# Kernel optimization log

Measured on AMD Instinct MI355X. Metric: run time of the kernel, lower is better.

## Reference

```python
import jax, jax.numpy as jnp
import numpy as np

DIM = 64
N = 10000
E = 40000


def setup_inputs() -> dict:
    key = jax.random.key(0)
    ks = jax.random.split(key, 16)
    def rn(k, shape, s):
        return jax.random.normal(k, shape, dtype=jnp.float32) * s
    inp = {}
    inp["x"] = jax.random.normal(ks[0], (N, 3), dtype=jnp.float32)
    inp["edge_attr"] = jax.random.uniform(ks[1], (E, 7), dtype=jnp.float32)
    inp["edge_index"] = jax.random.randint(ks[2], (2, E), 0, N)
    inp["batch"] = jnp.zeros((N,), dtype=jnp.int32)
    # lin0: Linear(3, dim)
    inp["lin0_w"] = rn(ks[3], (DIM, 3), 0.3)
    inp["lin0_b"] = jnp.zeros((DIM,), jnp.float32)
    # edge MLP: Linear(7, dim) -> ReLU -> Linear(dim, dim*dim)
    inp["em1_w"] = rn(ks[4], (DIM, 7), 0.3)
    inp["em1_b"] = jnp.zeros((DIM,), jnp.float32)
    inp["em2_w"] = rn(ks[5], (DIM * DIM, DIM), 0.05)
    inp["em2_b"] = jnp.zeros((DIM * DIM,), jnp.float32)
    # NNConv root weight [in, out] and bias
    inp["root_w"] = rn(ks[6], (DIM, DIM), 0.1)
    inp["conv_b"] = jnp.zeros((DIM,), jnp.float32)
    # GRU(dim, dim), gate order r, z, n
    inp["gru_wih"] = rn(ks[7], (3 * DIM, DIM), 0.1)
    inp["gru_whh"] = rn(ks[8], (3 * DIM, DIM), 0.1)
    inp["gru_bih"] = jnp.zeros((3 * DIM,), jnp.float32)
    inp["gru_bhh"] = jnp.zeros((3 * DIM,), jnp.float32)
    # Set2Set LSTM(2*dim, dim), gate order i, f, g, o
    inp["lstm_wih"] = rn(ks[9], (4 * DIM, 2 * DIM), 0.1)
    inp["lstm_whh"] = rn(ks[10], (4 * DIM, DIM), 0.1)
    inp["lstm_bih"] = jnp.zeros((4 * DIM,), jnp.float32)
    inp["lstm_bhh"] = jnp.zeros((4 * DIM,), jnp.float32)
    inp["lin1_w"] = rn(ks[11], (DIM, 2 * DIM), 0.1)
    inp["lin1_b"] = jnp.zeros((DIM,), jnp.float32)
    inp["lin3_w"] = rn(ks[12], (1, DIM), 0.1)
    inp["lin3_b"] = jnp.zeros((1,), jnp.float32)
    return inp


def _forward(x, edge_attr, lin0_w, lin0_b, em1_w, em1_b, em2_w, em2_b,
             root_w, conv_b, gru_wih, gru_whh, gru_bih, gru_bhh,
             lstm_wih, lstm_whh, lstm_bih, lstm_bhh,
             lin1_w, lin1_b, lin3_w, lin3_b, edge_index, batch):
    n = x.shape[0]
    dim = lin0_w.shape[0]
    src, dst = edge_index[0], edge_index[1]

    out = jax.nn.relu(x @ lin0_w.T + lin0_b)  # [N, dim]
    h = out                                   # GRU hidden state

    # Edge-conditioned weights depend only on edge_attr -> compute once.
    we = jax.nn.relu(edge_attr @ em1_w.T + em1_b) @ em2_w.T + em2_b
    we = we.reshape(-1, dim, dim)             # [E, dim, dim]

    deg = jax.ops.segment_sum(jnp.ones_like(src, dtype=x.dtype), dst, num_segments=n)
    inv_deg = jnp.where(deg > 0, 1.0 / jnp.maximum(deg, 1.0), 0.0)[:, None]

    for _ in range(6):
        # NNConv: per-edge matmul, scatter-mean, plus root transform
        msg = jnp.einsum('ei,eio->eo', out[src], we)            # [E, dim]
        agg = jax.ops.segment_sum(msg, dst, num_segments=n) * inv_deg
        m = jax.nn.relu(out @ root_w + agg + conv_b)            # [N, dim]
        # single-step GRU over nodes (seq_len=1, batch=N)
        gi = m @ gru_wih.T + gru_bih
        gh = h @ gru_whh.T + gru_bhh
        ir, iz, inew = jnp.split(gi, 3, axis=-1)
        hr, hz, hnew = jnp.split(gh, 3, axis=-1)
        r = jax.nn.sigmoid(ir + hr)
        z = jax.nn.sigmoid(iz + hz)
        ncand = jnp.tanh(inew + r * hnew)
        h = (1.0 - z) * ncand + z * h
        out = h

    # Set2Set pooling; single graph (batch is all zeros, pool.view(1,-1))
    q_star = jnp.zeros((1, 2 * dim), x.dtype)
    hl = jnp.zeros((1, dim), x.dtype)
    cl = jnp.zeros((1, dim), x.dtype)
    for _ in range(6):
        g = q_star @ lstm_wih.T + lstm_bih + hl @ lstm_whh.T + lstm_bhh
        gi_, gf_, gg_, go_ = jnp.split(g, 4, axis=-1)
        cl = jax.nn.sigmoid(gf_) * cl + jax.nn.sigmoid(gi_) * jnp.tanh(gg_)
        hl = jax.nn.sigmoid(go_) * jnp.tanh(cl)
        q = hl                                                  # [1, dim]
        e = jnp.einsum('nd,d->n', out, q[0])                    # attention logits
        a = jax.nn.softmax(e)                                   # softmax over the single graph
        r = jnp.einsum('n,nd->d', a, out)[None, :]              # readout [1, dim]
        q_star = jnp.concatenate([q, r], axis=-1)               # [1, 2*dim]

    pool = q_star.reshape(1, -1)
    hid = jax.nn.relu(pool @ lin1_w.T + lin1_b)
    return hid @ lin3_w.T + lin3_b                              # [1, 1]


def reference(x, edge_attr, edge_index, batch, lin0_w, lin0_b, em1_w, em1_b,
              em2_w, em2_b, root_w, conv_b, gru_wih, gru_whh, gru_bih, gru_bhh,
              lstm_wih, lstm_whh, lstm_bih, lstm_bhh, lin1_w, lin1_b, lin3_w, lin3_b):
    return _forward(x, edge_attr, lin0_w, lin0_b, em1_w, em1_b, em2_w, em2_b,
                    root_w, conv_b, gru_wih, gru_whh, gru_bih, gru_bhh,
                    lstm_wih, lstm_whh, lstm_bih, lstm_bhh,
                    lin1_w, lin1_b, lin3_w, lin3_b, edge_index, batch)
```

## Files before the change

### kernel.cpp

```cpp
#include <hip/hip_runtime.h>
#include <math.h>

#define NNODES 10000
#define NEDGES 40000
#define DIM 64
#define MC 4160
#define WS 200
#define AST2 72

typedef short bf16x8 __attribute__((ext_vector_type(8)));
typedef float floatx4 __attribute__((ext_vector_type(4)));

__device__ __forceinline__ float sigmoidf_(float x) { return 1.0f / (1.0f + expf(-x)); }

__device__ __forceinline__ unsigned short f2bf(float x) {
    unsigned int u = __float_as_uint(x);
    u += 0x7fffu + ((u >> 16) & 1u);
    return (unsigned short)(u >> 16);
}
__device__ __forceinline__ float bf2f(unsigned short h) {
    return __uint_as_float(((unsigned int)h) << 16);
}
__device__ __forceinline__ void write_split(unsigned short* __restrict__ p, int d, float v) {
    unsigned short hi = f2bf(v);
    unsigned short lo = f2bf(v - bf2f(hi));
    p[d] = hi;
    p[64 + d] = hi;
    p[128 + d] = lo;
}

__global__ __launch_bounds__(256) void k_prep(const float* __restrict__ x,
                                              const float* __restrict__ lin0_w,
                                              const float* __restrict__ lin0_b,
                                              float* __restrict__ out,
                                              unsigned short* __restrict__ Abf,
                                              const float* __restrict__ em2_w,
                                              const float* __restrict__ em2_b,
                                              unsigned short* __restrict__ Bbf,
                                              const float* __restrict__ root_w,
                                              const float* __restrict__ gwih,
                                              const float* __restrict__ gwhh,
                                              unsigned short* __restrict__ Wcat,
                                              const float* __restrict__ lwih,
                                              const float* __restrict__ lwhh,
                                              float* __restrict__ wcT,
                                              float* __restrict__ wrT,
                                              const int* __restrict__ ei,
                                              int* __restrict__ counts,
                                              float* __restrict__ deg) {
    const int b = blockIdx.x;
    const int tid = threadIdx.x;
    if (b < 2500) {
        int idx = b * 256 + tid;
        if (idx >= NNODES * 64) return;
        int n = idx >> 6, d = idx & 63;
        float a = lin0_b[d];
        a += x[n * 3 + 0] * lin0_w[d * 3 + 0];
        a += x[n * 3 + 1] * lin0_w[d * 3 + 1];
        a += x[n * 3 + 2] * lin0_w[d * 3 + 2];
        float v = fmaxf(a, 0.0f);
        out[idx] = v;
        write_split(Abf + (size_t)n * 192, d, v);
    } else if (b < 3540) {
        int idx = (b - 2500) * 256 + tid;
        if (idx >= 64 * MC) return;
        int c = idx >> 6, i = idx & 63;
        float v;
        if (c < 4096) {
            v = em2_w[((size_t)(i * 64 + (c >> 6))) * 64 + (c & 63)];
        } else {
            v = em2_b[i * 64 + (c - 4096)];
        }
        unsigned short hi = f2bf(v);
        unsigned short lo = f2bf(v - bf2f(hi));
        unsigned short* row = Bbf + (size_t)c * 192;
        row[i] = hi;
        row[64 + i] = lo;
        row[128 + i] = hi;
    } else if (b < 3652) {
        int idx = (b - 3540) * 256 + tid;
        if (idx >= 448 * 64) return;
        int r = idx >> 6, i = idx & 63;
        float v;
        if (r < 64) v = root_w[i * 64 + r];
        else if (r < 256) v = gwih[(r - 64) * 64 + i];
        else v = gwhh[(r - 256) * 64 + i];
        unsigned short hi = f2bf(v);
        unsigned short lo = f2bf(v - bf2f(hi));
        unsigned short* row = Wcat + (size_t)r * 192;
        row[i] = hi;
        row[64 + i] = lo;
        row[128 + i] = hi;
    } else if (b < 3780) {
        int idx = (b - 3652) * 256 + tid;
        if (idx < 64 * 256) {
            int k = idx >> 8, t = idx & 255;
            wcT[idx] = lwih[t * 128 + k] + lwhh[t * 64 + k];
        } else if (idx < 2 * 64 * 256) {
            int i2 = idx - 64 * 256;
            int k = i2 >> 8, t = i2 & 255;
            wrT[i2] = lwih[t * 128 + 64 + k];
        }
    } else {
        int e = (b - 3780) * 256 + tid;
        if (e < NEDGES) {
            atomicAdd(&counts[ei[e]], 1);
            atomicAdd(&deg[ei[NEDGES + e]], 1.0f);
        }
    }
}

__global__ __launch_bounds__(256) void k_scan(const int* __restrict__ counts,
                                              const float* __restrict__ deg,
                                              int* __restrict__ row_start,
                                              int* __restrict__ cursor,
                                              float* __restrict__ invd) {
    __shared__ int partial[256];
    const int tid = threadIdx.x;
    const int base = tid * 40;
    int local[40];
    int sum = 0;
#pragma unroll
    for (int i = 0; i < 40; ++i) {
        int idx = base + i;
        int v = (idx < NNODES) ? counts[idx] : 0;
        local[i] = sum;
        sum += v;
    }
    partial[tid] = sum;
    __syncthreads();
    for (int off = 1; off < 256; off <<= 1) {
        int t = (tid >= off) ? partial[tid - off] : 0;
        __syncthreads();
        partial[tid] += t;
        __syncthreads();
    }
    const int prev = (tid > 0) ? partial[tid - 1] : 0;
#pragma unroll
    for (int i = 0; i < 40; ++i) {
        int idx = base + i;
        if (idx < NNODES) {
            int rs = prev + local[i];
            row_start[idx] = rs;
            cursor[idx] = rs;
            float dg = deg[idx];
            invd[idx] = dg > 0.0f ? 1.0f / dg : 0.0f;
        }
    }
    if (tid == 255) row_start[NNODES] = partial[255];
}

__global__ __launch_bounds__(256) void k_edge(const int* __restrict__ ei,
                                              const float* __restrict__ ea,
                                              const float* __restrict__ w,
                                              const float* __restrict__ bvec,
                                              int* __restrict__ cursor,
                                              int* __restrict__ dst_s,
                                              float* __restrict__ h1s) {
    const int wv = threadIdx.x >> 6, lane = threadIdx.x & 63;
    const int e = blockIdx.x * 4 + wv;
    if (e >= NEDGES) return;
    int pos = 0;
    if (lane == 0) {
        int s = ei[e];
        pos = atomicAdd(&cursor[s], 1);
        dst_s[pos] = ei[NEDGES + e];
    }
    pos = __shfl(pos, 0);
    float a = bvec[lane];
#pragma unroll
    for (int j = 0; j < 7; ++j) a += ea[e * 7 + j] * w[lane * 7 + j];
    h1s[(size_t)pos * 64 + lane] = fmaxf(a, 0.0f);
}

__global__ __launch_bounds__(256) void k_gemmM(const unsigned short* __restrict__ Abf,
                                               const unsigned short* __restrict__ Bbf,
                                               unsigned short* __restrict__ Mb) {
    __shared__ __align__(16) unsigned short As[64 * AST2];
    __shared__ __align__(16) unsigned short Bs[64 * AST2];
    __shared__ __align__(16) float Cs[64 * 68];
    const int tid = threadIdx.x;
    const int col0 = blockIdx.x * 64;
    const int wave = tid >> 6, lane = tid & 63;
    const int mi = lane & 15, q = lane >> 4;
#pragma unroll
    for (int j = 0; j < 2; ++j) {
        int idx = tid + 256 * j;
        int r = idx >> 3, c8 = (idx & 7) * 8;
        *reinterpret_cast<uint4*>(&Bs[r * AST2 + c8]) =
            *reinterpret_cast<const uint4*>(&Bbf[(size_t)(col0 + r) * 192 + c8]);
    }
    for (int rt = 0; rt < 4; ++rt) {
        const int row0 = (blockIdx.y * 4 + rt) * 64;
#pragma unroll
        for (int j = 0; j < 2; ++j) {
            int idx = tid + 256 * j;
            int r = idx >> 3, c8 = (idx & 7) * 8;
            int ra = row0 + r;
            if (ra >= NNODES) ra = NNODES - 1;
            *reinterpret_cast<uint4*>(&As[r * AST2 + c8]) =
                *reinterpret_cast<const uint4*>(&Abf[(size_t)ra * 192 + c8]);
        }
        __syncthreads();
        floatx4 acc[4];
#pragma unroll
        for (int nt = 0; nt < 4; ++nt)
#pragma unroll
            for (int r = 0; r < 4; ++r) acc[nt][r] = 0.0f;
        const unsigned short* arow = &As[(wave * 16 + mi) * AST2 + q * 8];
#pragma unroll
        for (int ks = 0; ks < 2; ++ks) {
            bf16x8 a = *reinterpret_cast<const bf16x8*>(arow + ks * 32);
#pragma unroll
            for (int nt = 0; nt < 4; ++nt) {
                bf16x8 b = *reinterpret_cast<const bf16x8*>(&Bs[(nt * 16 + mi) * AST2 + ks * 32 + q * 8]);
                acc[nt] = __builtin_amdgcn_mfma_f32_16x16x32_bf16(a, b, acc[nt], 0, 0, 0);
            }
        }
        const int rl = wave * 16 + q * 4;
#pragma unroll
        for (int nt = 0; nt < 4; ++nt)
#pragma unroll
            for (int r = 0; r < 4; ++r)
                Cs[(rl + r) * 68 + nt * 16 + mi] = acc[nt][r];
        __syncthreads();
#pragma unroll
        for (int j = 0; j < 2; ++j) {
            int idx = tid + 256 * j;
            int r = idx >> 3, c8 = (idx & 7) * 8;
            int row = row0 + r;
            if (row < NNODES) {
                const float* src = &Cs[r * 68 + c8];
                unsigned int p0 = (unsigned int)f2bf(src[0]) | ((unsigned int)f2bf(src[1]) << 16);
                unsigned int p1 = (unsigned int)f2bf(src[2]) | ((unsigned int)f2bf(src[3]) << 16);
                unsigned int p2 = (unsigned int)f2bf(src[4]) | ((unsigned int)f2bf(src[5]) << 16);
                unsigned int p3 = (unsigned int)f2bf(src[6]) | ((unsigned int)f2bf(src[7]) << 16);
                *reinterpret_cast<uint4*>(&Mb[(size_t)row * MC + col0 + c8]) =
                    make_uint4(p0, p1, p2, p3);
            }
        }
        __syncthreads();
    }
}

__global__ __launch_bounds__(256) void k_msg(const unsigned short* __restrict__ Mb,
                                             const float* __restrict__ h1s,
                                             const int* __restrict__ row_start,
                                             const int* __restrict__ dst_s,
                                             float* __restrict__ agg) {
    const int w = threadIdx.x >> 6;
    const int o = threadIdx.x & 63;
    const int s = blockIdx.x * 4 + w;
    const int e0 = row_start[s], e1 = row_start[s + 1];
    if (e0 == e1) return;
    const unsigned short* mrow = Mb + (size_t)s * MC + o * 64;
    uint4 m[8];
#pragma unroll
    for (int j = 0; j < 8; ++j)
        m[j] = *reinterpret_cast<const uint4*>(mrow + j * 8);
    const float bias = bf2f(Mb[(size_t)s * MC + 4096 + o]);
    for (int e = e0; e < e1; ++e) {
        const float4* hv = reinterpret_cast<const float4*>(h1s + (size_t)e * 64);
        float acc = bias;
#pragma unroll
        for (int j = 0; j < 8; ++j) {
            float4 ha = hv[2 * j];
            float4 hb = hv[2 * j + 1];
            unsigned int u;
            u = m[j].x;
            acc += ha.x * __uint_as_float(u << 16) + ha.y * __uint_as_float(u & 0xffff0000u);
            u = m[j].y;
            acc += ha.z * __uint_as_float(u << 16) + ha.w * __uint_as_float(u & 0xffff0000u);
            u = m[j].z;
            acc += hb.x * __uint_as_float(u << 16) + hb.y * __uint_as_float(u & 0xffff0000u);
            u = m[j].w;
            acc += hb.z * __uint_as_float(u << 16) + hb.w * __uint_as_float(u & 0xffff0000u);
        }
        atomicAdd(&agg[(size_t)dst_s[e] * 64 + o], acc);
    }
}

__global__ __launch_bounds__(256) void k_node(float* __restrict__ agg,
                                              const float* __restrict__ invdeg,
                                              const unsigned short* __restrict__ Wcat,
                                              const float* __restrict__ conv_b,
                                              const float* __restrict__ bih,
                                              const float* __restrict__ bhh,
                                              float* __restrict__ out,
                                              unsigned short* __restrict__ Abf) {
    __shared__ unsigned short As[32 * WS];
    __shared__ unsigned short Ms[32 * WS];
    __shared__ float ho[32 * 68];
    const int tid = threadIdx.x;
    const int row0 = blockIdx.x * 32;
#pragma unroll
    for (int j = 0; j < 3; ++j) {
        int idx = tid + 256 * j;
        int r = idx / 24, jj = idx % 24;
        int ra = row0 + r; if (ra >= NNODES) ra = NNODES - 1;
        *reinterpret_cast<uint4*>(&As[r * WS + jj * 8]) =
            *reinterpret_cast<const uint4*>(&Abf[(size_t)ra * 192 + jj * 8]);
    }
#pragma unroll
    for (int j = 0; j < 2; ++j) {
        int idx = tid + 256 * j;
        int r = idx >> 4, c4 = (idx & 15) * 4;
        int ra = row0 + r; if (ra >= NNODES) ra = NNODES - 1;
        *reinterpret_cast<float4*>(&ho[r * 68 + c4]) =
            *reinterpret_cast<const float4*>(&out[(size_t)ra * 64 + c4]);
    }
    __syncthreads();
    const int wave = tid >> 6, lane = tid & 63;
    const int mi = lane & 15, q = lane >> 4;
    const int d = wave * 16 + mi;
    floatx4 gh[2][3];
#pragma unroll
    for (int rt = 0; rt < 2; ++rt)
#pragma unroll
        for (int g = 0; g < 3; ++g)
#pragma unroll
            for (int r = 0; r < 4; ++r) gh[rt][g][r] = 0.0f;
#pragma unroll
    for (int ks = 0; ks < 6; ++ks) {
        bf16x8 b[3];
#pragma unroll
        for (int g = 0; g < 3; ++g)
            b[g] = *reinterpret_cast<const bf16x8*>(&Wcat[(size_t)(256 + g * 64 + d) * 192 + ks * 32 + q * 8]);
#pragma unroll
        for (int rt = 0; rt < 2; ++rt) {
            bf16x8 a = *reinterpret_cast<const bf16x8*>(&As[(rt * 16 + mi) * WS + ks * 32 + q * 8]);
#pragma unroll
            for (int g = 0; g < 3; ++g)
                gh[rt][g] = __builtin_amdgcn_mfma_f32_16x16x32_bf16(a, b[g], gh[rt][g], 0, 0, 0);
        }
    }
    {
        floatx4 cm[2];
#pragma unroll
        for (int rt = 0; rt < 2; ++rt)
#pragma unroll
            for (int r = 0; r < 4; ++r) cm[rt][r] = 0.0f;
#pragma unroll
        for (int ks = 0; ks < 6; ++ks) {
            bf16x8 b = *reinterpret_cast<const bf16x8*>(&Wcat[(size_t)d * 192 + ks * 32 + q * 8]);
#pragma unroll
            for (int rt = 0; rt < 2; ++rt) {
                bf16x8 a = *reinterpret_cast<const bf16x8*>(&As[(rt * 16 + mi) * WS + ks * 32 + q * 8]);
                cm[rt] = __builtin_amdgcn_mfma_f32_16x16x32_bf16(a, b, cm[rt], 0, 0, 0);
            }
        }
        const float cb = conv_b[d];
#pragma unroll
        for (int rt = 0; rt < 2; ++rt) {
#pragma unroll
            for (int r = 0; r < 4; ++r) {
                int row = rt * 16 + q * 4 + r;
                int ra = row0 + row; int rc = (ra < NNODES) ? ra : NNODES - 1;
                float v = cm[rt][r] + agg[(size_t)rc * 64 + d] * invdeg[rc] + cb;
                if (ra < NNODES) agg[(size_t)ra * 64 + d] = 0.0f;
                v = fmaxf(v, 0.0f);
                unsigned short hi = f2bf(v);
                unsigned short lo = f2bf(v - bf2f(hi));
                Ms[row * WS + d] = hi;
                Ms[row * WS + 64 + d] = hi;
                Ms[row * WS + 128 + d] = lo;
            }
        }
    }
    __syncthreads();
    floatx4 gi[2][3];
#pragma unroll
    for (int rt = 0; rt < 2; ++rt)
#pragma unroll
        for (int g = 0; g < 3; ++g)
#pragma unroll
            for (int r = 0; r < 4; ++r) gi[rt][g][r] = 0.0f;
#pragma unroll
    for (int ks = 0; ks < 6; ++ks) {
        bf16x8 b[3];
#pragma unroll
        for (int g = 0; g < 3; ++g)
            b[g] = *reinterpret_cast<const bf16x8*>(&Wcat[(size_t)(64 + g * 64 + d) * 192 + ks * 32 + q * 8]);
#pragma unroll
        for (int rt = 0; rt < 2; ++rt) {
            bf16x8 a = *reinterpret_cast<const bf16x8*>(&Ms[(rt * 16 + mi) * WS + ks * 32 + q * 8]);
#pragma unroll
            for (int g = 0; g < 3; ++g)
                gi[rt][g] = __builtin_amdgcn_mfma_f32_16x16x32_bf16(a, b[g], gi[rt][g], 0, 0, 0);
        }
    }
    const float bi_r = bih[d], bi_z = bih[64 + d], bi_n = bih[128 + d];
    const float bh_r = bhh[d], bh_z = bhh[64 + d], bh_n = bhh[128 + d];
#pragma unroll
    for (int rt = 0; rt < 2; ++rt) {
#pragma unroll
        for (int r = 0; r < 4; ++r) {
            int row = rt * 16 + q * 4 + r;
            int ra = row0 + row;
            float rr = sigmoidf_(gi[rt][0][r] + bi_r + gh[rt][0][r] + bh_r);
            float zz = sigmoidf_(gi[rt][1][r] + bi_z + gh[rt][1][r] + bh_z);
            float nc = tanhf(gi[rt][2][r] + bi_n + rr * (gh[rt][2][r] + bh_n));
            float hn = (1.0f - zz) * nc + zz * ho[row * 68 + d];
            if (ra < NNODES) {
                out[(size_t)ra * 64 + d] = hn;
                write_split(Abf + (size_t)ra * 192, d, hn);
            }
        }
    }
}

__global__ __launch_bounds__(256) void k_step(const float* __restrict__ out,
                                              const float* __restrict__ wcT,
                                              const float* __restrict__ wrT,
                                              const float* __restrict__ bih,
                                              const float* __restrict__ bhh,
                                              float* __restrict__ hc,
                                              float* rs,
                                              int it) {
    __shared__ float outs[256 * 65];
    __shared__ float hl_s[64];
    __shared__ float qr[64];
    __shared__ float gsh[256];
    __shared__ float wsh[256];
    __shared__ float red[256];
    const int tid = threadIdx.x;
    const int n0 = blockIdx.x * 256;
#pragma unroll
    for (int j = 0; j < 16; ++j) {
        int idx = tid + 256 * j;
        int r = idx >> 4, c4 = (idx & 15) * 4;
        int n = n0 + r;
        float4 v = make_float4(0.0f, 0.0f, 0.0f, 0.0f);
        if (n < NNODES) v = *reinterpret_cast<const float4*>(&out[(size_t)n * 64 + c4]);
        outs[r * 65 + c4 + 0] = v.x;
        outs[r * 65 + c4 + 1] = v.y;
        outs[r * 65 + c4 + 2] = v.z;
        outs[r * 65 + c4 + 3] = v.w;
    }
    if (tid < 64) {
        hl_s[tid] = hc[it * 128 + tid];
        qr[tid] = (it > 0) ? rs[it * 68 + tid] / rs[it * 68 + 64] : 0.0f;
    }
    __syncthreads();
    float g0 = 0.0f, g1 = 0.0f, g2 = 0.0f, g3 = 0.0f;
#pragma unroll 4
    for (int k = 0; k < 64; k += 4) {
        g0 += hl_s[k + 0] * wcT[(k + 0) * 256 + tid] + qr[k + 0] * wrT[(k + 0) * 256 + tid];
        g1 += hl_s[k + 1] * wcT[(k + 1) * 256 + tid] + qr[k + 1] * wrT[(k + 1) * 256 + tid];
        g2 += hl_s[k + 2] * wcT[(k + 2) * 256 + tid] + qr[k + 2] * wrT[(k + 2) * 256 + tid];
        g3 += hl_s[k + 3] * wcT[(k + 3) * 256 + tid] + qr[k + 3] * wrT[(k + 3) * 256 + tid];
    }
    gsh[tid] = bih[tid] + bhh[tid] + ((g0 + g1) + (g2 + g3));
    __syncthreads();
    if (tid < 64) {
        float ig = sigmoidf_(gsh[tid]);
        float fg = sigmoidf_(gsh[64 + tid]);
        float gg = tanhf(gsh[128 + tid]);
        float og = sigmoidf_(gsh[192 + tid]);
        float c = fg * hc[it * 128 + 64 + tid] + ig * gg;
        float h = og * tanhf(c);
        hl_s[tid] = h;
        hc[(it + 1) * 128 + tid] = h;
        hc[(it + 1) * 128 + 64 + tid] = c;
    }
    __syncthreads();
    float w = 0.0f;
    if (n0 + tid < NNODES) {
        const float* row = &outs[tid * 65];
        float e0 = 0.0f, e1 = 0.0f, e2 = 0.0f, e3 = 0.0f;
#pragma unroll 8
        for (int k = 0; k < 64; k += 4) {
            e0 += row[k + 0] * hl_s[k + 0];
            e1 += row[k + 1] * hl_s[k + 1];
            e2 += row[k + 2] * hl_s[k + 2];
            e3 += row[k + 3] * hl_s[k + 3];
        }
        w = expf((e0 + e1) + (e2 + e3));
    }
    wsh[tid] = w;
    red[tid] = w;
    __syncthreads();
    for (int s = 128; s > 0; s >>= 1) {
        if (tid < s) red[tid] += red[tid + s];
        __syncthreads();
    }
    if (tid == 0) atomicAdd(&rs[(it + 1) * 68 + 64], red[0]);
    const int grp = tid >> 6, d = tid & 63;
    float a0 = 0.0f, a1 = 0.0f;
#pragma unroll 8
    for (int j = 0; j < 64; j += 2) {
        a0 += wsh[grp * 64 + j] * outs[(grp * 64 + j) * 65 + d];
        a1 += wsh[grp * 64 + j + 1] * outs[(grp * 64 + j + 1) * 65 + d];
    }
    atomicAdd(&rs[(it + 1) * 68 + d], a0 + a1);
}

__global__ __launch_bounds__(128) void k_out(const float* __restrict__ hc,
                                             const float* __restrict__ rs,
                                             const float* __restrict__ lin1_w,
                                             const float* __restrict__ lin1_b,
                                             const float* __restrict__ lin3_w,
                                             const float* __restrict__ lin3_b,
                                             float* __restrict__ dout) {
    __shared__ float qs[128];
    __shared__ float hs[64];
    int tid = threadIdx.x;
    qs[tid] = (tid < 64) ? hc[6 * 128 + tid] : rs[6 * 68 + (tid - 64)] / rs[6 * 68 + 64];
    __syncthreads();
    if (tid < 64) {
        float a = lin1_b[tid];
        for (int k = 0; k < 128; ++k) a += qs[k] * lin1_w[tid * 128 + k];
        hs[tid] = fmaxf(a, 0.0f);
    }
    __syncthreads();
    if (tid == 0) {
        float a = lin3_b[0];
        for (int k = 0; k < 64; ++k) a += hs[k] * lin3_w[k];
        dout[0] = a;
    }
}

extern "C" void kernel_launch(void* const* d_in, const int* in_sizes, int n_in,
                              void* d_out, int out_size, void* d_ws, size_t ws_size,
                              hipStream_t stream) {
    const float* x         = (const float*)d_in[0];
    const float* edge_attr = (const float*)d_in[1];
    const int*   ei        = (const int*)d_in[2];
    const float* lin0_w    = (const float*)d_in[4];
    const float* lin0_b    = (const float*)d_in[5];
    const float* em1_w     = (const float*)d_in[6];
    const float* em1_b     = (const float*)d_in[7];
    const float* em2_w     = (const float*)d_in[8];
    const float* em2_b     = (const float*)d_in[9];
    const float* root_w    = (const float*)d_in[10];
    const float* conv_b    = (const float*)d_in[11];
    const float* gru_wih   = (const float*)d_in[12];
    const float* gru_whh   = (const float*)d_in[13];
    const float* gru_bih   = (const float*)d_in[14];
    const float* gru_bhh   = (const float*)d_in[15];
    const float* lstm_wih  = (const float*)d_in[16];
    const float* lstm_whh  = (const float*)d_in[17];
    const float* lstm_bih  = (const float*)d_in[18];
    const float* lstm_bhh  = (const float*)d_in[19];
    const float* lin1_w    = (const float*)d_in[20];
    const float* lin1_b    = (const float*)d_in[21];
    const float* lin3_w    = (const float*)d_in[22];
    const float* lin3_b    = (const float*)d_in[23];

    float* ws = (float*)d_ws;
    size_t off = 0;
    unsigned short* Mb   = (unsigned short*)(ws + off); off += (size_t)NNODES * MC / 2;
    unsigned short* Abf  = (unsigned short*)(ws + off); off += (size_t)NNODES * 192 / 2;
    unsigned short* Bbf  = (unsigned short*)(ws + off); off += (size_t)MC * 192 / 2;
    unsigned short* Wcat = (unsigned short*)(ws + off); off += (size_t)448 * 192 / 2;
    float* h1s   = ws + off; off += (size_t)NEDGES * 64;
    float* outb  = ws + off; off += (size_t)NNODES * 64;
    float* agg   = ws + off; off += (size_t)NNODES * 64;
    float* deg   = ws + off; off += NNODES;
    int*   counts    = (int*)(ws + off); off += NNODES;
    int*   cursor    = (int*)(ws + off); off += NNODES;
    int*   row_start = (int*)(ws + off); off += NNODES + 4;
    int*   dst_s     = (int*)(ws + off); off += NEDGES;
    float* invd  = ws + off; off += NNODES;
    float* wcT   = ws + off; off += 64 * 256;
    float* wrT   = ws + off; off += 64 * 256;
    float* rs    = ws + off; off += 7 * 68;
    float* hc    = ws + off; off += 7 * 128;

    hipMemsetAsync(deg, 0, 3 * NNODES * sizeof(float), stream);
    hipMemsetAsync(agg, 0, (size_t)NNODES * 64 * sizeof(float), stream);
    hipMemsetAsync(rs, 0, (7 * 68 + 7 * 128) * sizeof(float), stream);
    k_prep<<<3937, 256, 0, stream>>>(x, lin0_w, lin0_b, outb, Abf,
                                     em2_w, em2_b, Bbf,
                                     root_w, gru_wih, gru_whh, Wcat,
                                     lstm_wih, lstm_whh, wcT, wrT,
                                     ei, counts, deg);
    k_scan<<<1, 256, 0, stream>>>(counts, deg, row_start, cursor, invd);
    k_edge<<<10000, 256, 0, stream>>>(ei, edge_attr, em1_w, em1_b, cursor, dst_s, h1s);

    for (int t = 0; t < 6; ++t) {
        k_gemmM<<<dim3(65, 40), 256, 0, stream>>>(Abf, Bbf, Mb);
        k_msg<<<2500, 256, 0, stream>>>(Mb, h1s, row_start, dst_s, agg);
        k_node<<<313, 256, 0, stream>>>(agg, invd, Wcat, conv_b, gru_bih, gru_bhh,
                                        outb, Abf);
    }

    for (int it = 0; it < 6; ++it)
        k_step<<<40, 256, 0, stream>>>(outb, wcT, wrT, lstm_bih, lstm_bhh, hc, rs, it);
    k_out<<<1, 128, 0, stream>>>(hc, rs, lin1_w, lin1_b, lin3_w, lin3_b, (float*)d_out);
}
```

Measured before the change: 700.3 us.

## Replace node-weight GEMM plus message kernel with fused per-edge outer-product MFMA conv

Instead of precomputing a per-source-node matrix M (N x 4160) via a GEMM and then applying it per edge, each block of 128 edges forms the outer product of the source node feature and the edge hidden vector on the fly as bf16 MFMA A operands. These are multiplied against the em2 weight (plus the bias block) streamed through double-buffered shared memory, and the results are atomically added into agg. This avoids writing and reading the large N x 4160 intermediate every iteration and merges two launches into one. In exchange it does 4x more MFMA work (per edge rather than per node) and drops the hi/lo split precision, using a single bf16 product for inputs and weights.

```diff
diff --git a/kernel.cpp b/kernel.cpp
--- a/kernel.cpp
+++ b/kernel.cpp
@@ -4,9 +4,11 @@
 #define NNODES 10000
 #define NEDGES 40000
 #define DIM 64
-#define MC 4160
 #define WS 200
-#define AST2 72
+#define EB 128
+#define H1S 68
+#define OTS 72
+#define BSS 72
 
 typedef short bf16x8 __attribute__((ext_vector_type(8)));
 typedef float floatx4 __attribute__((ext_vector_type(4)));
@@ -36,7 +38,7 @@
                                               unsigned short* __restrict__ Abf,
                                               const float* __restrict__ em2_w,
                                               const float* __restrict__ em2_b,
-                                              unsigned short* __restrict__ Bbf,
+                                              unsigned short* __restrict__ Bek,
                                               const float* __restrict__ root_w,
                                               const float* __restrict__ gwih,
                                               const float* __restrict__ gwhh,
@@ -63,20 +65,10 @@
         write_split(Abf + (size_t)n * 192, d, v);
     } else if (b < 3540) {
         int idx = (b - 2500) * 256 + tid;
-        if (idx >= 64 * MC) return;
-        int c = idx >> 6, i = idx & 63;
-        float v;
-        if (c < 4096) {
-            v = em2_w[((size_t)(i * 64 + (c >> 6))) * 64 + (c & 63)];
-        } else {
-            v = em2_b[i * 64 + (c - 4096)];
-        }
-        unsigned short hi = f2bf(v);
-        unsigned short lo = f2bf(v - bf2f(hi));
-        unsigned short* row = Bbf + (size_t)c * 192;
-        row[i] = hi;
-        row[64 + i] = lo;
-        row[128 + i] = hi;
+        if (idx >= 4160 * 64) return;
+        int r = idx >> 6, k = idx & 63;
+        float v = (r < 4096) ? em2_w[(size_t)r * 64 + k] : em2_b[k * 64 + (r - 4096)];
+        Bek[idx] = f2bf(v);
     } else if (b < 3652) {
         int idx = (b - 3540) * 256 + tid;
         if (idx >= 448 * 64) return;
@@ -155,6 +147,7 @@
                                               const float* __restrict__ w,
                                               const float* __restrict__ bvec,
                                               int* __restrict__ cursor,
+                                              int* __restrict__ src_s,
                                               int* __restrict__ dst_s,
                                               float* __restrict__ h1s) {
     const int wv = threadIdx.x >> 6, lane = threadIdx.x & 63;
@@ -164,6 +157,7 @@
     if (lane == 0) {
         int s = ei[e];
         pos = atomicAdd(&cursor[s], 1);
+        src_s[pos] = s;
         dst_s[pos] = ei[NEDGES + e];
     }
     pos = __shfl(pos, 0);
@@ -173,110 +167,90 @@
     h1s[(size_t)pos * 64 + lane] = fmaxf(a, 0.0f);
 }
 
-__global__ __launch_bounds__(256) void k_gemmM(const unsigned short* __restrict__ Abf,
-                                               const unsigned short* __restrict__ Bbf,
-                                               unsigned short* __restrict__ Mb) {
-    __shared__ __align__(16) unsigned short As[64 * AST2];
-    __shared__ __align__(16) unsigned short Bs[64 * AST2];
-    __shared__ __align__(16) float Cs[64 * 68];
+__global__ __launch_bounds__(512) void k_econv(const float* __restrict__ out,
+                                               const float* __restrict__ h1s,
+                                               const unsigned short* __restrict__ Bek,
+                                               const int* __restrict__ src_s,
+                                               const int* __restrict__ dst_s,
+                                               float* __restrict__ agg) {
+    __shared__ __align__(16) float h1f[EB * H1S];
+    __shared__ __align__(16) unsigned short out_t[EB * OTS];
+    __shared__ __align__(16) unsigned short Bs[2][64 * BSS];
     const int tid = threadIdx.x;
-    const int col0 = blockIdx.x * 64;
-    const int wave = tid >> 6, lane = tid & 63;
+    const int w = tid >> 6, lane = tid & 63;
     const int mi = lane & 15, q = lane >> 4;
-#pragma unroll
-    for (int j = 0; j < 2; ++j) {
-        int idx = tid + 256 * j;
-        int r = idx >> 3, c8 = (idx & 7) * 8;
-        *reinterpret_cast<uint4*>(&Bs[r * AST2 + c8]) =
-            *reinterpret_cast<const uint4*>(&Bbf[(size_t)(col0 + r) * 192 + c8]);
-    }
-    for (int rt = 0; rt < 4; ++rt) {
-        const int row0 = (blockIdx.y * 4 + rt) * 64;
-#pragma unroll
-        for (int j = 0; j < 2; ++j) {
-            int idx = tid + 256 * j;
-            int r = idx >> 3, c8 = (idx & 7) * 8;
-            int ra = row0 + r;
-            if (ra >= NNODES) ra = NNODES - 1;
-            *reinterpret_cast<uint4*>(&As[r * AST2 + c8]) =
-                *reinterpret_cast<const uint4*>(&Abf[(size_t)ra * 192 + c8]);
+    const int e0 = blockIdx.x * EB;
+#pragma unroll
+    for (int j = 0; j < 4; ++j) {
+        int idx = tid + 512 * j;
+        int r = idx >> 4, c4 = (idx & 15) * 4;
+        int e = e0 + r;
+        float4 h = make_float4(0.0f, 0.0f, 0.0f, 0.0f);
+        float4 o4 = make_float4(0.0f, 0.0f, 0.0f, 0.0f);
+        if (e < NEDGES) {
+            h = *reinterpret_cast<const float4*>(&h1s[(size_t)e * 64 + c4]);
+            int s = src_s[e];
+            o4 = *reinterpret_cast<const float4*>(&out[(size_t)s * 64 + c4]);
+        }
+        *reinterpret_cast<float4*>(&h1f[r * H1S + c4]) = h;
+        unsigned int p0 = (unsigned int)f2bf(o4.x) | ((unsigned int)f2bf(o4.y) << 16);
+        unsigned int p1 = (unsigned int)f2bf(o4.z) | ((unsigned int)f2bf(o4.w) << 16);
+        *reinterpret_cast<uint2*>(&out_t[r * OTS + c4]) = make_uint2(p0, p1);
+    }
+    {
+        int r = tid >> 3, c8 = (tid & 7) * 8;
+        *reinterpret_cast<uint4*>(&Bs[0][r * BSS + c8]) =
+            *reinterpret_cast<const uint4*>(&Bek[(size_t)r * 64 + c8]);
+    }
+    __syncthreads();
+    floatx4 acc[4];
+#pragma unroll
+    for (int nt = 0; nt < 4; ++nt)
+#pragma unroll
+        for (int r = 0; r < 4; ++r) acc[nt][r] = 0.0f;
+    const int m = w * 16 + mi;
+    int buf = 0;
+    for (int c = 0; c <= 64; ++c) {
+        if (c < 64) {
+            int r = tid >> 3, c8 = (tid & 7) * 8;
+            *reinterpret_cast<uint4*>(&Bs[buf ^ 1][r * BSS + c8]) =
+                *reinterpret_cast<const uint4*>(&Bek[(size_t)(c + 1) * 4096 + r * 64 + c8]);
+        }
+        bf16x8 a0, a1;
+        if (c < 64) {
+            const float s = bf2f(out_t[m * OTS + c]);
+            const float* hp = &h1f[m * H1S + q * 8];
+#pragma unroll
+            for (int j = 0; j < 8; ++j) {
+                a0[j] = (short)f2bf(s * hp[j]);
+                a1[j] = (short)f2bf(s * hp[32 + j]);
+            }
+        } else {
+            a0 = *reinterpret_cast<const bf16x8*>(&out_t[m * OTS + q * 8]);
+            a1 = *reinterpret_cast<const bf16x8*>(&out_t[m * OTS + 32 + q * 8]);
+        }
+#pragma unroll
+        for (int nt = 0; nt < 4; ++nt) {
+            bf16x8 b0 = *reinterpret_cast<const bf16x8*>(&Bs[buf][(nt * 16 + mi) * BSS + q * 8]);
+            bf16x8 b1 = *reinterpret_cast<const bf16x8*>(&Bs[buf][(nt * 16 + mi) * BSS + 32 + q * 8]);
+            acc[nt] = __builtin_amdgcn_mfma_f32_16x16x32_bf16(a0, b0, acc[nt], 0, 0, 0);
+            acc[nt] = __builtin_amdgcn_mfma_f32_16x16x32_bf16(a1, b1, acc[nt], 0, 0, 0);
         }
         __syncthreads();
-        floatx4 acc[4];
-#pragma unroll
-        for (int nt = 0; nt < 4; ++nt)
-#pragma unroll
-            for (int r = 0; r < 4; ++r) acc[nt][r] = 0.0f;
-        const unsigned short* arow = &As[(wave * 16 + mi) * AST2 + q * 8];
-#pragma unroll
-        for (int ks = 0; ks < 2; ++ks) {
-            bf16x8 a = *reinterpret_cast<const bf16x8*>(arow + ks * 32);
-#pragma unroll
-            for (int nt = 0; nt < 4; ++nt) {
-                bf16x8 b = *reinterpret_cast<const bf16x8*>(&Bs[(nt * 16 + mi) * AST2 + ks * 32 + q * 8]);
-                acc[nt] = __builtin_amdgcn_mfma_f32_16x16x32_bf16(a, b, acc[nt], 0, 0, 0);
-            }
-        }
-        const int rl = wave * 16 + q * 4;
-#pragma unroll
-        for (int nt = 0; nt < 4; ++nt)
-#pragma unroll
-            for (int r = 0; r < 4; ++r)
-                Cs[(rl + r) * 68 + nt * 16 + mi] = acc[nt][r];
-        __syncthreads();
-#pragma unroll
-        for (int j = 0; j < 2; ++j) {
-            int idx = tid + 256 * j;
-            int r = idx >> 3, c8 = (idx & 7) * 8;
-            int row = row0 + r;
-            if (row < NNODES) {
-                const float* src = &Cs[r * 68 + c8];
-                unsigned int p0 = (unsigned int)f2bf(src[0]) | ((unsigned int)f2bf(src[1]) << 16);
-                unsigned int p1 = (unsigned int)f2bf(src[2]) | ((unsigned int)f2bf(src[3]) << 16);
-                unsigned int p2 = (unsigned int)f2bf(src[4]) | ((unsigned int)f2bf(src[5]) << 16);
-                unsigned int p3 = (unsigned int)f2bf(src[6]) | ((unsigned int)f2bf(src[7]) << 16);
-                *reinterpret_cast<uint4*>(&Mb[(size_t)row * MC + col0 + c8]) =
-                    make_uint4(p0, p1, p2, p3);
-            }
-        }
-        __syncthreads();
-    }
-}
-
-__global__ __launch_bounds__(256) void k_msg(const unsigned short* __restrict__ Mb,
-                                             const float* __restrict__ h1s,
-                                             const int* __restrict__ row_start,
-                                             const int* __restrict__ dst_s,
-                                             float* __restrict__ agg) {
-    const int w = threadIdx.x >> 6;
-    const int o = threadIdx.x & 63;
-    const int s = blockIdx.x * 4 + w;
-    const int e0 = row_start[s], e1 = row_start[s + 1];
-    if (e0 == e1) return;
-    const unsigned short* mrow = Mb + (size_t)s * MC + o * 64;
-    uint4 m[8];
-#pragma unroll
-    for (int j = 0; j < 8; ++j)
-        m[j] = *reinterpret_cast<const uint4*>(mrow + j * 8);
-    const float bias = bf2f(Mb[(size_t)s * MC + 4096 + o]);
-    for (int e = e0; e < e1; ++e) {
-        const float4* hv = reinterpret_cast<const float4*>(h1s + (size_t)e * 64);
-        float acc = bias;
-#pragma unroll
-        for (int j = 0; j < 8; ++j) {
-            float4 ha = hv[2 * j];
-            float4 hb = hv[2 * j + 1];
-            unsigned int u;
-            u = m[j].x;
-            acc += ha.x * __uint_as_float(u << 16) + ha.y * __uint_as_float(u & 0xffff0000u);
-            u = m[j].y;
-            acc += ha.z * __uint_as_float(u << 16) + ha.w * __uint_as_float(u & 0xffff0000u);
-            u = m[j].z;
-            acc += hb.x * __uint_as_float(u << 16) + hb.y * __uint_as_float(u & 0xffff0000u);
-            u = m[j].w;
-            acc += hb.z * __uint_as_float(u << 16) + hb.w * __uint_as_float(u & 0xffff0000u);
-        }
-        atomicAdd(&agg[(size_t)dst_s[e] * 64 + o], acc);
+        buf ^= 1;
+    }
+#pragma unroll
+    for (int nt = 0; nt < 4; ++nt)
+#pragma unroll
+        for (int r = 0; r < 4; ++r)
+            h1f[(w * 16 + q * 4 + r) * H1S + nt * 16 + mi] = acc[nt][r];
+    __syncthreads();
+#pragma unroll
+    for (int rr = 0; rr < 16; ++rr) {
+        int row = w * 16 + rr;
+        int e = e0 + row;
+        if (e < NEDGES)
+            atomicAdd(&agg[(size_t)dst_s[e] * 64 + lane], h1f[row * H1S + lane]);
     }
 }
 
@@ -549,9 +523,8 @@
 
     float* ws = (float*)d_ws;
     size_t off = 0;
-    unsigned short* Mb   = (unsigned short*)(ws + off); off += (size_t)NNODES * MC / 2;
     unsigned short* Abf  = (unsigned short*)(ws + off); off += (size_t)NNODES * 192 / 2;
-    unsigned short* Bbf  = (unsigned short*)(ws + off); off += (size_t)MC * 192 / 2;
+    unsigned short* Bek  = (unsigned short*)(ws + off); off += (size_t)4160 * 64 / 2;
     unsigned short* Wcat = (unsigned short*)(ws + off); off += (size_t)448 * 192 / 2;
     float* h1s   = ws + off; off += (size_t)NEDGES * 64;
     float* outb  = ws + off; off += (size_t)NNODES * 64;
@@ -560,6 +533,7 @@
     int*   counts    = (int*)(ws + off); off += NNODES;
     int*   cursor    = (int*)(ws + off); off += NNODES;
     int*   row_start = (int*)(ws + off); off += NNODES + 4;
+    int*   src_s     = (int*)(ws + off); off += NEDGES;
     int*   dst_s     = (int*)(ws + off); off += NEDGES;
     float* invd  = ws + off; off += NNODES;
     float* wcT   = ws + off; off += 64 * 256;
@@ -571,16 +545,16 @@
     hipMemsetAsync(agg, 0, (size_t)NNODES * 64 * sizeof(float), stream);
     hipMemsetAsync(rs, 0, (7 * 68 + 7 * 128) * sizeof(float), stream);
     k_prep<<<3937, 256, 0, stream>>>(x, lin0_w, lin0_b, outb, Abf,
-                                     em2_w, em2_b, Bbf,
+                                     em2_w, em2_b, Bek,
                                      root_w, gru_wih, gru_whh, Wcat,
                                      lstm_wih, lstm_whh, wcT, wrT,
                                      ei, counts, deg);
     k_scan<<<1, 256, 0, stream>>>(counts, deg, row_start, cursor, invd);
-    k_edge<<<10000, 256, 0, stream>>>(ei, edge_attr, em1_w, em1_b, cursor, dst_s, h1s);
-
+    k_edge<<<10000, 256, 0, stream>>>(ei, edge_attr, em1_w, em1_b, cursor, src_s, dst_s, h1s);
+
+    const int neb = (NEDGES + EB - 1) / EB;
     for (int t = 0; t < 6; ++t) {
-        k_gemmM<<<dim3(65, 40), 256, 0, stream>>>(Abf, Bbf, Mb);
-        k_msg<<<2500, 256, 0, stream>>>(Mb, h1s, row_start, dst_s, agg);
+        k_econv<<<neb, 512, 0, stream>>>(outb, h1s, Bek, src_s, dst_s, agg);
         k_node<<<313, 256, 0, stream>>>(agg, invd, Wcat, conv_b, gru_bih, gru_bhh,
                                         outb, Abf);
     }
```

Result: slower. 739.3 us (+5.6%).
